# Kernel optimization log

Hardware: AMD Instinct MI355X
Metric: run time of the kernel (lower is better)

The kernel has to match this reference:

```python
import jax, jax.numpy as jnp
import numpy as np

N_X, N_UNITS, N_Y, N_U = 64, 256, 32, 64
BATCH = 32768


def setup_inputs() -> dict:
    key = jax.random.key(0)
    ks = jax.random.split(key, 10)
    nz = 2 * N_X + N_UNITS
    return {
        "u": jax.random.normal(ks[0], (BATCH, N_U, 1), dtype=jnp.float32),
        "x0": jax.random.normal(ks[1], (BATCH, N_X, 1), dtype=jnp.float32),
        # learned parameters (scaled down so H stays well-conditioned and tanh unsaturated)
        "B_2": 0.1 * jax.random.normal(ks[2], (N_X, N_U), dtype=jnp.float32),
        "C_2": 0.1 * jax.random.normal(ks[3], (N_Y, N_X), dtype=jnp.float32),
        "D_12": 0.1 * jax.random.normal(ks[4], (N_UNITS, N_U), dtype=jnp.float32),
        "D_21": 0.1 * jax.random.normal(ks[5], (N_Y, N_UNITS), dtype=jnp.float32),
        "b": 0.1 * jax.random.normal(ks[6], (N_X + N_UNITS + N_Y, 1), dtype=jnp.float32),
        "X": (1.0 / np.sqrt(nz)) * jax.random.normal(ks[7], (nz, nz), dtype=jnp.float32),
        "Y1": 0.1 * jax.random.normal(ks[8], (N_X, N_X), dtype=jnp.float32),
        # fixed IQC multipliers (train_qsr=False): Q nsd, R=I so Rinv=I; S stored transposed
        "S_t": 0.1 * jax.random.normal(ks[9], (N_U, N_Y), dtype=jnp.float32),
        "Q": -jnp.eye(N_Y, dtype=jnp.float32),
        "Rinv": jnp.eye(N_U, dtype=jnp.float32),
    }


def _constrained_weights(B_2, C_2, D_12, D_21, X, S_t, Q, Rinv):
    """Port of REN.updateConstrainedWeights (train_qsr=False). Returns C_1, D_11, lam."""
    n_x, n_units = B_2.shape[0], D_12.shape[0]
    n_y = C_2.shape[0]
    nz = 2 * n_x + n_units
    C2_ = S_t @ C_2                       # [n_u, n_x]
    D21_ = S_t @ D_21 - D_12.T            # [n_u, n_units]
    H = X.T @ X + 1e-3 * jnp.eye(nz, dtype=X.dtype)
    lT1 = jnp.concatenate([C2_.T, D21_.T, B_2], axis=0)          # [nz, n_u]
    H = H + lT1 @ Rinv @ lT1.T
    lT2 = jnp.concatenate([C_2.T, D_21.T, jnp.zeros((n_x, n_y), dtype=X.dtype)], axis=0)
    H = H - lT2 @ Q @ lT2.T
    H_21 = H[n_x:n_x + n_units, :n_x]
    H_22 = H[n_x:n_x + n_units, n_x:n_x + n_units]
    C_1 = -H_21                           # [n_units, n_x]
    lam = 0.5 * jnp.diag(H_22)            # Lambda diagonal, > 0 since H is PD
    # L = tril(-(H_22 - diag(H_22))) == -strictly_lower(H_22)
    D_11 = -jnp.tril(H_22, k=-1)          # strictly lower triangular [n_units, n_units]
    return C_1, D_11, lam


def _forward(u, x0, B_2, C_2, D_12, D_21, b, X, Y1, S_t, Q, Rinv):
    n_x, n_units = B_2.shape[0], D_12.shape[0]
    C_1, D_11, lam = _constrained_weights(B_2, C_2, D_12, D_21, X, S_t, Q, Rinv)
    u2 = u[:, :, 0]                       # [B, n_u]
    x2 = x0[:, :, 0]                      # [B, n_x]
    b_w = b[n_x:n_x + n_units, 0]         # [n_units]
    b_y = b[n_x + n_units:, 0]            # [n_y]
    # precompute the non-recurrent part of the pre-activation for all units
    v = x2 @ C_1.T + u2 @ D_12.T + b_w    # [B, n_units]
    # NOTE: the source uses D_11 row (i_unit - 1), not i_unit (faithful to original code).
    # For i=0 the source uses term2 = 0; D_11 is strictly lower so the full-row dot
    # against the partially-filled w (zeros beyond index i) matches D_11[i-1, :i] @ w[:i].
    Drows = jnp.concatenate([jnp.zeros((1, n_units), dtype=D_11.dtype), D_11[:-1]], axis=0)
    batch = u2.shape[0]

    def step(w, i):
        wi = jnp.tanh((v[:, i] + w @ Drows[i]) / lam[i])   # [B]
        w = w.at[:, i].set(wi)
        return w, None

    w0 = jnp.zeros((batch, n_units), dtype=v.dtype)
    w, _ = jax.lax.scan(step, w0, jnp.arange(n_units))
    y = x2 @ C_2.T + w @ D_21.T + b_y     # [B, n_y]
    return y[:, :, None]                  # [B, n_y, 1]


def reference(u, x0, B_2, C_2, D_12, D_21, b, X, Y1, S_t, Q, Rinv):
    return _forward(u, x0, B_2, C_2, D_12, D_21, b, X, Y1, S_t, Q, Rinv)
```

## Files before the change

kernel.cpp:

```cpp
#include <hip/hip_runtime.h>
#include <hip/hip_bf16.h>

typedef __attribute__((ext_vector_type(8))) short short8;
typedef __attribute__((ext_vector_type(4))) float floatx4;

#define MFMA16 __builtin_amdgcn_mfma_f32_16x16x32_bf16

__device__ inline unsigned short bf16_rn(float f) {
    return (unsigned short)((__float_as_uint(f) + 0x8000u) >> 16);
}
__device__ inline short8 pack8(const float* v) {
    short8 r;
#pragma unroll
    for (int j = 0; j < 8; j++) r[j] = (short)bf16_rn(v[j]);
    return r;
}

__global__ __launch_bounds__(64) void ren_prep13(
    const float* __restrict__ B2, const float* __restrict__ C2,
    const float* __restrict__ D12, const float* __restrict__ D21,
    const float* __restrict__ St, const float* __restrict__ Q,
    const float* __restrict__ Rinv,
    float* __restrict__ lT1, float* __restrict__ t1,
    float* __restrict__ lT2, float* __restrict__ t2,
    unsigned short* __restrict__ Wvb, unsigned short* __restrict__ C2b,
    unsigned short* __restrict__ D21b)
{
    const int t = threadIdx.x;
    const int blk = blockIdx.x;
    if (blk >= 384) {
        const int id = (blk - 384) * 64 + t;
        if (id < 16384) {
            Wvb[(id >> 6) * 128 + 64 + (id & 63)] = bf16_rn(D12[id]);
        } else if (id < 16384 + 2048) {
            C2b[id - 16384] = bf16_rn(C2[id - 16384]);
        } else if (id < 16384 + 2048 + 8192) {
            D21b[id - 18432] = bf16_rn(D21[id - 18432]);
        }
        return;
    }

    __shared__ float stl[64 * 33];
    __shared__ float colbuf[32];
    __shared__ float s1[64];

    const int r = blk;
    const int c = t;
#pragma unroll
    for (int j = 0; j < 32; j++) {
        const int id = j * 64 + t;
        stl[(id >> 5) * 33 + (id & 31)] = St[id];
    }
    if (t < 32)
        colbuf[t] = (r < 64) ? C2[t * 64 + r]
                  : (r < 320 ? D21[t * 256 + (r - 64)] : 0.f);
    __syncthreads();

    float v1;
    if (r < 64) {
        float s = 0.f;
#pragma unroll
        for (int p = 0; p < 32; p++) s += stl[c * 33 + p] * colbuf[p];
        v1 = s;
    } else if (r < 320) {
        float s = 0.f;
#pragma unroll
        for (int p = 0; p < 32; p++) s += stl[c * 33 + p] * colbuf[p];
        v1 = s - D12[(r - 64) * 64 + c];
    } else {
        v1 = B2[(r - 320) * 64 + c];
    }
    s1[c] = v1;
    lT1[r * 64 + c] = v1;
    if (c < 32) {
        const float v2 = (r < 320) ? colbuf[c] : 0.f;
        lT2[r * 32 + c] = v2;
    }
    __syncthreads();

    float a = 0.f;
#pragma unroll
    for (int k = 0; k < 64; k++) a += s1[k] * Rinv[k * 64 + c];
    t1[r * 64 + c] = a;

    if (c < 32) {
        float bq = 0.f;
#pragma unroll
        for (int k = 0; k < 32; k++) bq += colbuf[k] * Q[k * 32 + c];
        t2[r * 32 + c] = bq;
    }
}

__global__ __launch_bounds__(320) void ren_prep2(
    const float* __restrict__ X,
    const float* __restrict__ lT1, const float* __restrict__ t1,
    const float* __restrict__ lT2, const float* __restrict__ t2,
    unsigned short* __restrict__ Wvb, unsigned short* __restrict__ Drowsb,
    float* __restrict__ Dtri, float* __restrict__ lamg)
{
    __shared__ float xcol[384];
    const int c = threadIdx.x;
    const int i = blockIdx.x;
    for (int t = c; t < 384; t += 320) xcol[t] = X[t * 384 + 64 + i];
    __syncthreads();

    float f0 = 0.f, f1 = 0.f, f2 = 0.f, f3 = 0.f;
    float ac[8], au[8], bc8[8], bu[8];
#pragma unroll
    for (int kk = 0; kk < 8; kk++) { ac[kk] = X[kk * 384 + c]; au[kk] = xcol[kk]; }
    for (int k0 = 0; k0 < 384; k0 += 16) {
#pragma unroll
        for (int kk = 0; kk < 8; kk++) {
            bc8[kk] = X[(k0 + 8 + kk) * 384 + c]; bu[kk] = xcol[k0 + 8 + kk];
        }
        f0 += au[0] * ac[0]; f1 += au[1] * ac[1];
        f2 += au[2] * ac[2]; f3 += au[3] * ac[3];
        f0 += au[4] * ac[4]; f1 += au[5] * ac[5];
        f2 += au[6] * ac[6]; f3 += au[7] * ac[7];
        if (k0 + 16 < 384) {
#pragma unroll
            for (int kk = 0; kk < 8; kk++) {
                ac[kk] = X[(k0 + 16 + kk) * 384 + c]; au[kk] = xcol[k0 + 16 + kk];
            }
        }
        f0 += bu[0] * bc8[0]; f1 += bu[1] * bc8[1];
        f2 += bu[2] * bc8[2]; f3 += bu[3] * bc8[3];
        f0 += bu[4] * bc8[4]; f1 += bu[5] * bc8[5];
        f2 += bu[6] * bc8[6]; f3 += bu[7] * bc8[7];
    }

    const float* __restrict__ t1r = t1 + (64 + i) * 64;
    const float* __restrict__ l1r = lT1 + c * 64;
#pragma unroll
    for (int m4 = 0; m4 < 16; m4++) {
        const float4 lv = *(const float4*)(l1r + m4 * 4);
        f0 += t1r[m4 * 4 + 0] * lv.x; f1 += t1r[m4 * 4 + 1] * lv.y;
        f2 += t1r[m4 * 4 + 2] * lv.z; f3 += t1r[m4 * 4 + 3] * lv.w;
    }
    const float* __restrict__ t2r = t2 + (64 + i) * 32;
    const float* __restrict__ l2r = lT2 + c * 32;
#pragma unroll
    for (int m4 = 0; m4 < 8; m4++) {
        const float4 lv = *(const float4*)(l2r + m4 * 4);
        f0 -= t2r[m4 * 4 + 0] * lv.x; f1 -= t2r[m4 * 4 + 1] * lv.y;
        f2 -= t2r[m4 * 4 + 2] * lv.z; f3 -= t2r[m4 * 4 + 3] * lv.w;
    }
    float acc = (f0 + f1) + (f2 + f3) + (((64 + i) == c) ? 0.001f : 0.f);

    if (c < 64) {
        Wvb[i * 128 + c] = bf16_rn(-acc);
    } else {
        const int cb = c - 64;
        if (i == 0 && cb < 16) Dtri[cb] = 0.f;
        if (cb == i) lamg[i] = 5.7707801635558536f / acc;
        if (i < 255) {
            const float dv = (cb <= i - 1) ? -acc : 0.f;
            Drowsb[(i + 1) * 256 + cb] = bf16_rn(dv);
            if (((i + 1) >> 4) == (cb >> 4))
                Dtri[((i + 1) >> 4) * 256 + ((i + 1) & 15) * 16 + (cb & 15)] = dv;
        } else {
            Drowsb[cb] = 0;
        }
    }
}

__global__ __launch_bounds__(64) void ren_main(
    const float* __restrict__ u, const float* __restrict__ x0,
    const float* __restrict__ b,
    const unsigned short* __restrict__ Wvb,
    const unsigned short* __restrict__ Drowsb,
    const float* __restrict__ Dtri,
    const float* __restrict__ lamg,
    const unsigned short* __restrict__ C2b,
    const unsigned short* __restrict__ D21b,
    float* __restrict__ out)
{
    __shared__ float buf[16][20];
    __shared__ float dblk[256];
    __shared__ float lamsh[256];
    __shared__ float bsh[256];

    const int L = threadIdx.x;
    const int col = L & 15;
    const int quad = L >> 4;
    const int row0 = blockIdx.x * 16;

#pragma unroll
    for (int j = 0; j < 4; j++) {
        lamsh[j * 64 + L] = lamg[j * 64 + L];
        bsh[j * 64 + L]   = b[64 + j * 64 + L];
    }

    short8 zf[4];
#pragma unroll
    for (int c = 0; c < 4; c++) {
        const float* p = (c < 2 ? x0 : u) + (long)(row0 + col) * 64 + (c & 1) * 32 + quad * 8;
        float t[8];
        *(float4*)&t[0] = *(const float4*)p;
        *(float4*)&t[4] = *(const float4*)(p + 4);
        zf[c] = pack8(t);
    }

    const short8 zero8 = {0, 0, 0, 0, 0, 0, 0, 0};
    short8 wf[8];
#pragma unroll
    for (int c = 0; c < 8; c++) wf[c] = zero8;

    short8 vf[2][4], hf[2][8], yc[4];
    float4 dt = *(const float4*)(Dtri + 4 * L);
#pragma unroll
    for (int c = 0; c < 4; c++)
        vf[0][c] = *(const short8*)(Wvb + col * 128 + c * 32 + quad * 8);
#pragma unroll
    for (int c = 0; c < 8; c++) { hf[0][c] = zero8; hf[1][c] = zero8; }

#pragma unroll
    for (int n = 0; n < 16; n++) {
        const int cur = n & 1, nxt = cur ^ 1;

        *(float4*)&dblk[4 * L] = dt;

        if (n < 15) {
            dt = *(const float4*)(Dtri + (n + 1) * 256 + 4 * L);
#pragma unroll
            for (int c = 0; c < 4; c++)
                vf[nxt][c] = *(const short8*)(Wvb + (16 * (n + 1) + col) * 128 + c * 32 + quad * 8);
#pragma unroll
            for (int c = 0; c < 8; c++)
                if (c < ((n + 2) >> 1))
                    hf[nxt][c] = *(const short8*)(Drowsb + (16 * (n + 1) + col) * 256 + c * 32 + quad * 8);
        } else {
            yc[0] = *(const short8*)(C2b + col * 64 + quad * 8);
            yc[1] = *(const short8*)(C2b + col * 64 + 32 + quad * 8);
            yc[2] = *(const short8*)(C2b + (16 + col) * 64 + quad * 8);
            yc[3] = *(const short8*)(C2b + (16 + col) * 64 + 32 + quad * 8);
        }

        floatx4 acc0 = {0.f, 0.f, 0.f, 0.f}, acc1 = {0.f, 0.f, 0.f, 0.f};
        acc0 = MFMA16(zf[0], vf[cur][0], acc0, 0, 0, 0);
        acc1 = MFMA16(zf[1], vf[cur][1], acc1, 0, 0, 0);
        acc0 = MFMA16(zf[2], vf[cur][2], acc0, 0, 0, 0);
        acc1 = MFMA16(zf[3], vf[cur][3], acc1, 0, 0, 0);
#pragma unroll
        for (int c = 0; c < 8; c++)
            if (c < ((n + 1) >> 1)) {
                if (c & 1) acc1 = MFMA16(wf[c], hf[cur][c], acc1, 0, 0, 0);
                else       acc0 = MFMA16(wf[c], hf[cur][c], acc0, 0, 0, 0);
            }

        const float bwv = bsh[16 * n + col];
#pragma unroll
        for (int r = 0; r < 4; r++)
            buf[quad * 4 + r][col] = acc0[r] + acc1[r] + bwv;

        float vl[16], lmv[16];
#pragma unroll
        for (int p4 = 0; p4 < 4; p4++) {
            *(float4*)&vl[p4 * 4]  = *(const float4*)&buf[col][p4 * 4];
            *(float4*)&lmv[p4 * 4] = *(const float4*)&lamsh[16 * n + p4 * 4];
        }

        float wl[16];
#pragma unroll
        for (int q = 0; q < 16; q++) wl[q] = 0.f;
#pragma unroll
        for (int q = 0; q < 16; q++) {
            float aa = vl[q], ab = 0.f;
            const int nb = (q >= 2) ? ((q + 2) >> 2) : 0;
#pragma unroll
            for (int p4 = 0; p4 < nb; p4++) {
                const float4 d4 = *(const float4*)&dblk[q * 16 + p4 * 4];
                aa += d4.x * wl[p4 * 4 + 0];
                ab += d4.y * wl[p4 * 4 + 1];
                aa += d4.z * wl[p4 * 4 + 2];
                ab += d4.w * wl[p4 * 4 + 3];
            }
            float tt = (aa + ab) * lmv[q];
            tt = fminf(44.f, fmaxf(-44.f, tt));
            const float e = __builtin_amdgcn_exp2f(tt);
            wl[q] = 1.f - 2.f * __builtin_amdgcn_rcpf(e + 1.f);
        }

        {
            const short8 nf = pack8(&wl[(quad & 1) * 8]);
            const int cc = n >> 1;
            if ((n & 1) == 0) wf[cc] = (quad < 2) ? nf : zero8;
            else if (quad >= 2) wf[cc] = nf;
        }
    }

    floatx4 y0 = {0.f, 0.f, 0.f, 0.f}, y1 = {0.f, 0.f, 0.f, 0.f};
    y0 = MFMA16(zf[0], yc[0], y0, 0, 0, 0);
    y1 = MFMA16(zf[0], yc[2], y1, 0, 0, 0);
    y0 = MFMA16(zf[1], yc[1], y0, 0, 0, 0);
    y1 = MFMA16(zf[1], yc[3], y1, 0, 0, 0);
#pragma unroll
    for (int c = 0; c < 8; c++) {
        const short8 b0 = *(const short8*)(D21b + col * 256 + c * 32 + quad * 8);
        const short8 b1 = *(const short8*)(D21b + (16 + col) * 256 + c * 32 + quad * 8);
        y0 = MFMA16(wf[c], b0, y0, 0, 0, 0);
        y1 = MFMA16(wf[c], b1, y1, 0, 0, 0);
    }
    const float by0 = b[320 + col];
    const float by1 = b[336 + col];
#pragma unroll
    for (int r = 0; r < 4; r++) {
        out[(long)(row0 + quad * 4 + r) * 32 + col]      = y0[r] + by0;
        out[(long)(row0 + quad * 4 + r) * 32 + 16 + col] = y1[r] + by1;
    }
}

extern "C" void kernel_launch(void* const* d_in, const int* in_sizes, int n_in,
                              void* d_out, int out_size, void* d_ws, size_t ws_size,
                              hipStream_t stream)
{
    const float* u    = (const float*)d_in[0];
    const float* x0   = (const float*)d_in[1];
    const float* B2   = (const float*)d_in[2];
    const float* C2   = (const float*)d_in[3];
    const float* D12  = (const float*)d_in[4];
    const float* D21  = (const float*)d_in[5];
    const float* b    = (const float*)d_in[6];
    const float* X    = (const float*)d_in[7];
    const float* St   = (const float*)d_in[9];
    const float* Q    = (const float*)d_in[10];
    const float* Rinv = (const float*)d_in[11];
    float* out = (float*)d_out;

    float* ws     = (float*)d_ws;
    float* lT1    = ws;
    float* t1     = lT1 + 384 * 64;
    float* lT2    = t1 + 384 * 64;
    float* t2     = lT2 + 384 * 32;
    float* lamg   = t2 + 384 * 32;
    float* Dtri   = lamg + 256;
    unsigned short* Drowsb = (unsigned short*)(Dtri + 16 * 256);
    unsigned short* Wvb    = Drowsb + 256 * 256;
    unsigned short* C2b    = Wvb + 256 * 128;
    unsigned short* D21b   = C2b + 32 * 64;

    ren_prep13<<<dim3(800), dim3(64), 0, stream>>>(B2, C2, D12, D21, St, Q, Rinv,
                                                   lT1, t1, lT2, t2, Wvb, C2b, D21b);
    ren_prep2<<<dim3(256), dim3(320), 0, stream>>>(X, lT1, t1, lT2, t2,
                                                   Wvb, Drowsb, Dtri, lamg);

    const int batch = in_sizes[0] / 64;
    ren_main<<<dim3(batch / 16), dim3(64), 0, stream>>>(u, x0, b, Wvb, Drowsb,
                                                        Dtri, lamg, C2b, D21b, out);
}
```

Measured before the change: 146.3 us.

## Solve unit recurrence two units at a time using pair-interleaved D layout

The shifted-row structure (row i uses D_11 row i-1, so each unit depends only on units two or more before it) lets each 16-unit block be solved in 8 steps of two independent units. The serial dependency chain per block is roughly halved. The prep kernel now writes the diagonal D blocks in a pair-interleaved layout, so one float4 load gives two coefficients for each of the two rows. The tanh argument clamp and the separate lambda register array are dropped in favour of fma chains and float2 lambda loads. Removing the clamp relies on exp2/rcp saturating correctly at inf and 0.

After: 142.2 us. 1.03x faster.

```diff
diff --git a/kernel.cpp b/kernel.cpp
--- a/kernel.cpp
+++ b/kernel.cpp
@@ -96,7 +96,7 @@
     const float* __restrict__ lT1, const float* __restrict__ t1,
     const float* __restrict__ lT2, const float* __restrict__ t2,
     unsigned short* __restrict__ Wvb, unsigned short* __restrict__ Drowsb,
-    float* __restrict__ Dtri, float* __restrict__ lamg)
+    float* __restrict__ Dpair, float* __restrict__ lamg)
 {
     __shared__ float xcol[384];
     const int c = threadIdx.x;
@@ -151,13 +151,15 @@
         Wvb[i * 128 + c] = bf16_rn(-acc);
     } else {
         const int cb = c - 64;
-        if (i == 0 && cb < 16) Dtri[cb] = 0.f;
         if (cb == i) lamg[i] = 5.7707801635558536f / acc;
         if (i < 255) {
             const float dv = (cb <= i - 1) ? -acc : 0.f;
             Drowsb[(i + 1) * 256 + cb] = bf16_rn(dv);
-            if (((i + 1) >> 4) == (cb >> 4))
-                Dtri[((i + 1) >> 4) * 256 + ((i + 1) & 15) * 16 + (cb & 15)] = dv;
+            const int row = i + 1;
+            if ((row >> 4) == (cb >> 4)) {
+                const int q = row & 15, p = cb & 15;
+                Dpair[(row >> 4) * 256 + (q >> 1) * 32 + p * 2 + (q & 1)] = dv;
+            }
         } else {
             Drowsb[cb] = 0;
         }
@@ -169,7 +171,7 @@
     const float* __restrict__ b,
     const unsigned short* __restrict__ Wvb,
     const unsigned short* __restrict__ Drowsb,
-    const float* __restrict__ Dtri,
+    const float* __restrict__ Dpair,
     const float* __restrict__ lamg,
     const unsigned short* __restrict__ C2b,
     const unsigned short* __restrict__ D21b,
@@ -207,7 +209,7 @@
     for (int c = 0; c < 8; c++) wf[c] = zero8;
 
     short8 vf[2][4], hf[2][8], yc[4];
-    float4 dt = *(const float4*)(Dtri + 4 * L);
+    float4 dt = *(const float4*)(Dpair + 4 * L);
 #pragma unroll
     for (int c = 0; c < 4; c++)
         vf[0][c] = *(const short8*)(Wvb + col * 128 + c * 32 + quad * 8);
@@ -221,7 +223,7 @@
         *(float4*)&dblk[4 * L] = dt;
 
         if (n < 15) {
-            dt = *(const float4*)(Dtri + (n + 1) * 256 + 4 * L);
+            dt = *(const float4*)(Dpair + (n + 1) * 256 + 4 * L);
 #pragma unroll
             for (int c = 0; c < 4; c++)
                 vf[nxt][c] = *(const short8*)(Wvb + (16 * (n + 1) + col) * 128 + c * 32 + quad * 8);
@@ -253,32 +255,28 @@
         for (int r = 0; r < 4; r++)
             buf[quad * 4 + r][col] = acc0[r] + acc1[r] + bwv;
 
-        float vl[16], lmv[16];
-#pragma unroll
-        for (int p4 = 0; p4 < 4; p4++) {
-            *(float4*)&vl[p4 * 4]  = *(const float4*)&buf[col][p4 * 4];
-            *(float4*)&lmv[p4 * 4] = *(const float4*)&lamsh[16 * n + p4 * 4];
-        }
+        float vl[16];
+#pragma unroll
+        for (int p4 = 0; p4 < 4; p4++)
+            *(float4*)&vl[p4 * 4] = *(const float4*)&buf[col][p4 * 4];
 
         float wl[16];
 #pragma unroll
-        for (int q = 0; q < 16; q++) wl[q] = 0.f;
-#pragma unroll
-        for (int q = 0; q < 16; q++) {
-            float aa = vl[q], ab = 0.f;
-            const int nb = (q >= 2) ? ((q + 2) >> 2) : 0;
-#pragma unroll
-            for (int p4 = 0; p4 < nb; p4++) {
-                const float4 d4 = *(const float4*)&dblk[q * 16 + p4 * 4];
-                aa += d4.x * wl[p4 * 4 + 0];
-                ab += d4.y * wl[p4 * 4 + 1];
-                aa += d4.z * wl[p4 * 4 + 2];
-                ab += d4.w * wl[p4 * 4 + 3];
+        for (int t = 0; t < 8; t++) {
+            float ax = vl[2 * t], ay = vl[2 * t + 1];
+#pragma unroll
+            for (int p4 = 0; p4 < t; p4++) {
+                const float4 d4 = *(const float4*)&dblk[t * 32 + p4 * 4];
+                ax = fmaf(d4.x, wl[2 * p4],     ax);
+                ay = fmaf(d4.y, wl[2 * p4],     ay);
+                ax = fmaf(d4.z, wl[2 * p4 + 1], ax);
+                ay = fmaf(d4.w, wl[2 * p4 + 1], ay);
             }
-            float tt = (aa + ab) * lmv[q];
-            tt = fminf(44.f, fmaxf(-44.f, tt));
-            const float e = __builtin_amdgcn_exp2f(tt);
-            wl[q] = 1.f - 2.f * __builtin_amdgcn_rcpf(e + 1.f);
+            const float2 lm = *(const float2*)&lamsh[16 * n + 2 * t];
+            const float e0 = __builtin_amdgcn_exp2f(ax * lm.x);
+            const float e1 = __builtin_amdgcn_exp2f(ay * lm.y);
+            wl[2 * t]     = 1.f - 2.f * __builtin_amdgcn_rcpf(e0 + 1.f);
+            wl[2 * t + 1] = 1.f - 2.f * __builtin_amdgcn_rcpf(e1 + 1.f);
         }
 
         {
@@ -333,8 +331,8 @@
     float* lT2    = t1 + 384 * 64;
     float* t2     = lT2 + 384 * 32;
     float* lamg   = t2 + 384 * 32;
-    float* Dtri   = lamg + 256;
-    unsigned short* Drowsb = (unsigned short*)(Dtri + 16 * 256);
+    float* Dpair  = lamg + 256;
+    unsigned short* Drowsb = (unsigned short*)(Dpair + 16 * 256);
     unsigned short* Wvb    = Drowsb + 256 * 256;
     unsigned short* C2b    = Wvb + 256 * 128;
     unsigned short* D21b   = C2b + 32 * 64;
@@ -342,9 +340,9 @@
     ren_prep13<<<dim3(800), dim3(64), 0, stream>>>(B2, C2, D12, D21, St, Q, Rinv,
                                                    lT1, t1, lT2, t2, Wvb, C2b, D21b);
     ren_prep2<<<dim3(256), dim3(320), 0, stream>>>(X, lT1, t1, lT2, t2,
-                                                   Wvb, Drowsb, Dtri, lamg);
+                                                   Wvb, Drowsb, Dpair, lamg);
 
     const int batch = in_sizes[0] / 64;
     ren_main<<<dim3(batch / 16), dim3(64), 0, stream>>>(u, x0, b, Wvb, Drowsb,
-                                                        Dtri, lamg, C2b, D21b, out);
-}
+                                                        Dpair, lamg, C2b, D21b, out);
+}
```
